# Kernel tuning notes

Hardware: AMD Instinct MI355X
Metric: run time of the kernel (lower is better)

## Reference

```python
import jax, jax.numpy as jnp
import numpy as np
from jax.scipy.special import erfinv

N_CHUNKS = 64
D = 128          # input_dim
O = 256          # output_dim
B = 4096         # batch (batch_last)
P = D // 2       # number of 2D pairs

def get_borders_cdf_grid(n):
    # CDF (Gaussian-quantile) spaced grid borders; clip probs to keep endpoints finite
    p = jnp.clip(jnp.arange(n + 1, dtype=jnp.float32) / n, 0.5 / n, 1.0 - 0.5 / n)
    return jnp.sqrt(2.0) * erfinv(2.0 * p - 1.0)

BORDERS = get_borders_cdf_grid(N_CHUNKS)  # (n_chunks+1,)


def setup_inputs() -> dict:
    key = jax.random.key(0)
    ks = jax.random.split(key, 5)
    s = 1.0 / np.sqrt(D)
    return {
        "x": jax.random.normal(ks[0], (D, B), dtype=jnp.float32),
        "weight_lmKAN": jnp.ones((1,), dtype=jnp.float32),
        "apply_relu_linear": 1,
        "func_parameter": jax.random.uniform(ks[1], (N_CHUNKS + 1, N_CHUNKS + 1, O, P), minval=-s, maxval=s, dtype=jnp.float32),
        "scale_parameters": jnp.ones((D,), dtype=jnp.float32),
        "bias_parameters": jnp.zeros((D,), dtype=jnp.float32),
        "W_linear": jax.random.uniform(ks[2], (O, D), minval=-s, maxval=s, dtype=jnp.float32),
        "bias_linear": jax.random.uniform(ks[3], (O,), minval=-s, maxval=s, dtype=jnp.float32),
    }


def lmkan_2d(fp, x):
    """2D bucketized grid lookup + bilinear interpolation.
    fp: (G, G, O, P) with G = n_chunks+1; x: (D, B) -> out (O, B)."""
    n = fp.shape[0] - 1
    pairs = x.reshape(P, 2, -1)                      # adjacent-channel pairs
    eps = 1e-6
    x1 = jnp.clip(pairs[:, 0], BORDERS[0], BORDERS[-1] - eps)  # (P, B)
    x2 = jnp.clip(pairs[:, 1], BORDERS[0], BORDERS[-1] - eps)
    i = jnp.clip(jnp.searchsorted(BORDERS, x1, side='right') - 1, 0, n - 1)
    j = jnp.clip(jnp.searchsorted(BORDERS, x2, side='right') - 1, 0, n - 1)
    t1 = (x1 - BORDERS[i]) / (BORDERS[i + 1] - BORDERS[i])      # (P, B) in [0,1)
    t2 = (x2 - BORDERS[j]) / (BORDERS[j + 1] - BORDERS[j])
    pidx = jnp.arange(P)[:, None]                    # (P, 1) -> broadcasts to (P, B)

    def corner(ii, jj, w):
        g = fp[ii, jj, :, pidx]                      # gather -> (P, B, O)
        return jnp.einsum('pb,pbo->ob', w, g)

    return (corner(i,     j,     (1.0 - t1) * (1.0 - t2))
          + corner(i + 1, j,     t1 * (1.0 - t2))
          + corner(i,     j + 1, (1.0 - t1) * t2)
          + corner(i + 1, j + 1, t1 * t2))


def reference(x, weight_lmKAN, apply_relu_linear, func_parameter, scale_parameters, bias_parameters, W_linear, bias_linear):
    # relu_last=True branch of the original forward
    linear_out = W_linear @ x + bias_linear[:, None]         # (O, B)
    if apply_relu_linear:
        linear_out = jax.nn.relu(linear_out)
    xs = x * scale_parameters[:, None] + bias_parameters[:, None]  # apply_scale / apply_bias
    # apply_tanh=False
    lmkan_out = lmkan_2d(func_parameter, xs)                 # (O, B)
    return 1.0 * linear_out + weight_lmKAN * lmkan_out
```

## Files before the change

### kernel.cpp

```cpp
#include <hip/hip_runtime.h>
#include <hip/hip_fp16.h>


#define NB 4096
#define ND 128
#define NO 256
#define NP 64
#define NG 65
#define PANEL 16384

__device__ __forceinline__ int bsearch65(const float* B, float v) {
  int lo = 0, hi = 65;
  while (lo < hi) {
    int m = (lo + hi) >> 1;
    if (B[m] <= v) lo = m + 1; else hi = m;
  }
  int i = lo - 1;
  return i < 0 ? 0 : (i > 63 ? 63 : i);
}

__global__ __launch_bounds__(128) void lmkan_transpose(
    const float* __restrict__ src, __half* __restrict__ dst) {
  const int panel = blockIdx.x;
  const int t = threadIdx.x;
  const float* s = src + (size_t)panel * PANEL;
  __half* d = dst + (size_t)panel * PANEL;
  const int o0 = 2 * t;
  const float4* ra = reinterpret_cast<const float4*>(s + (size_t)o0 * 64);
  const float4* rb = reinterpret_cast<const float4*>(s + (size_t)(o0 + 1) * 64);
#pragma unroll 4
  for (int pc = 0; pc < 16; ++pc) {
    float4 a = ra[pc];
    float4 b = rb[pc];
    *reinterpret_cast<__half2*>(d + (size_t)(4 * pc + 0) * NO + o0) = __floats2half2_rn(a.x, b.x);
    *reinterpret_cast<__half2*>(d + (size_t)(4 * pc + 1) * NO + o0) = __floats2half2_rn(a.y, b.y);
    *reinterpret_cast<__half2*>(d + (size_t)(4 * pc + 2) * NO + o0) = __floats2half2_rn(a.z, b.z);
    *reinterpret_cast<__half2*>(d + (size_t)(4 * pc + 3) * NO + o0) = __floats2half2_rn(a.w, b.w);
  }
}

__device__ __forceinline__ void fma8(float acc[8], float w, uint4 v) {
  const __half2* h = reinterpret_cast<const __half2*>(&v);
#pragma unroll
  for (int k = 0; k < 4; ++k) {
    float2 f = __half22float2(h[k]);
    acc[2 * k]     = fmaf(w, f.x, acc[2 * k]);
    acc[2 * k + 1] = fmaf(w, f.y, acc[2 * k + 1]);
  }
}

__global__ __launch_bounds__(256) void lmkan_gather4(
    const float* __restrict__ x, const float* __restrict__ scale,
    const float* __restrict__ biasp, const float* __restrict__ W,
    const float* __restrict__ bias_l, const float* __restrict__ wlm_p,
    const int* __restrict__ relu_p, const __half* __restrict__ fpt,
    float* __restrict__ out) {
  const int b = blockIdx.x;
  const int t = threadIdx.x;
  const int w = t >> 6;
  const int l = t & 63;
  const int h = l >> 5;
  const int L = l & 31;

  __shared__ float borders[66];
  __shared__ __align__(16) float xcol[ND];
  __shared__ int pbase[NP];
  __shared__ float4 pw[NP];
  __shared__ float lm[4][NO];

  if (t < 65) {
    float pk = fminf(fmaxf((float)t * (1.0f / 64.0f), 0.0078125f), 0.9921875f);
    borders[t] = 1.41421356237309515f * erfinvf(2.0f * pk - 1.0f);
  }
  if (t < ND) xcol[t] = x[(size_t)t * NB + b];
  __syncthreads();

  if (t < NP) {
    const int p = t;
    float x1 = xcol[2 * p]     * scale[2 * p]     + biasp[2 * p];
    float x2 = xcol[2 * p + 1] * scale[2 * p + 1] + biasp[2 * p + 1];
    const float lo = borders[0];
    const float hi = borders[64] - 1e-6f;
    x1 = fminf(fmaxf(x1, lo), hi);
    x2 = fminf(fmaxf(x2, lo), hi);
    int i = bsearch65(borders, x1);
    int j = bsearch65(borders, x2);
    float t1 = (x1 - borders[i]) / (borders[i + 1] - borders[i]);
    float t2 = (x2 - borders[j]) / (borders[j + 1] - borders[j]);
    pbase[p] = i * NG + j;
    pw[p] = make_float4((1.0f - t1) * (1.0f - t2),
                        t1 * (1.0f - t2),
                        (1.0f - t1) * t2,
                        t1 * t2);
  }
  __syncthreads();

  float acc[8] = {0, 0, 0, 0, 0, 0, 0, 0};
  const int p0 = w * 16;
#pragma unroll 8
  for (int pi = 0; pi < 16; ++pi) {
    const int p = p0 + pi;
    const int base = pbase[p] + h * NG;
    const float4 wv = pw[p];
    const float wA = h ? wv.y : wv.x;
    const float wB = h ? wv.w : wv.z;
    const __half* q = fpt + ((size_t)base * NP + p) * NO + 8 * L;
    uint4 v0 = *reinterpret_cast<const uint4*>(q);
    uint4 v1 = *reinterpret_cast<const uint4*>(q + PANEL);
    fma8(acc, wA, v0);
    fma8(acc, wB, v1);
  }
#pragma unroll
  for (int k = 0; k < 8; ++k) acc[k] += __shfl_xor(acc[k], 32, 64);
  if (l < 32) {
#pragma unroll
    for (int k = 0; k < 8; ++k) lm[w][8 * L + k] = acc[k];
  }
  __syncthreads();

  const int o = t;
  float lmsum = lm[0][o] + lm[1][o] + lm[2][o] + lm[3][o];
  const float4* wr = reinterpret_cast<const float4*>(W + (size_t)o * ND);
  const float4* xc4 = reinterpret_cast<const float4*>(xcol);
  float s = 0.0f;
#pragma unroll 8
  for (int d4 = 0; d4 < ND / 4; ++d4) {
    float4 wv = wr[d4];
    float4 xv = xc4[d4];
    s = fmaf(wv.x, xv.x, s);
    s = fmaf(wv.y, xv.y, s);
    s = fmaf(wv.z, xv.z, s);
    s = fmaf(wv.w, xv.w, s);
  }
  s += bias_l[o];
  if (relu_p[0]) s = fmaxf(s, 0.0f);
  out[(size_t)o * NB + b] = s + wlm_p[0] * lmsum;
}

__global__ __launch_bounds__(64) void lmkan_gather_direct(
    const float* __restrict__ x, const float* __restrict__ scale,
    const float* __restrict__ biasp, const float* __restrict__ W,
    const float* __restrict__ bias_l, const float* __restrict__ wlm_p,
    const int* __restrict__ relu_p, const float* __restrict__ fp,
    float* __restrict__ out) {
  const int b = blockIdx.x;
  const int t = threadIdx.x;

  __shared__ float borders[66];
  __shared__ __align__(16) float xcol[ND];
  __shared__ int pbase[NP];
  __shared__ float4 pw[NP];

  for (int k = t; k < 65; k += 64) {
    float pk = fminf(fmaxf((float)k * (1.0f / 64.0f), 0.0078125f), 0.9921875f);
    borders[k] = 1.41421356237309515f * erfinvf(2.0f * pk - 1.0f);
  }
  xcol[t]      = x[(size_t)t * NB + b];
  xcol[t + 64] = x[(size_t)(t + 64) * NB + b];
  __syncthreads();

  {
    const int p = t;
    float x1 = xcol[2 * p]     * scale[2 * p]     + biasp[2 * p];
    float x2 = xcol[2 * p + 1] * scale[2 * p + 1] + biasp[2 * p + 1];
    const float lo = borders[0];
    const float hi = borders[64] - 1e-6f;
    x1 = fminf(fmaxf(x1, lo), hi);
    x2 = fminf(fmaxf(x2, lo), hi);
    int i = bsearch65(borders, x1);
    int j = bsearch65(borders, x2);
    float t1 = (x1 - borders[i]) / (borders[i + 1] - borders[i]);
    float t2 = (x2 - borders[j]) / (borders[j + 1] - borders[j]);
    pbase[p] = i * NG + j;
    pw[p] = make_float4((1.0f - t1) * (1.0f - t2), t1 * (1.0f - t2),
                        (1.0f - t1) * t2, t1 * t2);
  }
  __syncthreads();

  float acc[4] = {0, 0, 0, 0};
  for (int p = 0; p < NP; ++p) {
    int base = pbase[p];
    float4 wv = pw[p];
#pragma unroll
    for (int k = 0; k < 4; ++k) {
      size_t r = ((size_t)base * NO + (4 * t + k)) * NP + p;
      acc[k] += wv.x * fp[r] + wv.y * fp[r + 65 * PANEL] +
                wv.z * fp[r + PANEL] + wv.w * fp[r + 66 * PANEL];
    }
  }

  const float wlm = wlm_p[0];
  const int rl = relu_p[0];
  const float4* xc4 = reinterpret_cast<const float4*>(xcol);
#pragma unroll
  for (int k = 0; k < 4; ++k) {
    const int o = 4 * t + k;
    const float4* wr = reinterpret_cast<const float4*>(W + (size_t)o * ND);
    float s = 0.0f;
#pragma unroll 8
    for (int d4 = 0; d4 < ND / 4; ++d4) {
      float4 wv = wr[d4];
      float4 xv = xc4[d4];
      s = fmaf(wv.x, xv.x, s);
      s = fmaf(wv.y, xv.y, s);
      s = fmaf(wv.z, xv.z, s);
      s = fmaf(wv.w, xv.w, s);
    }
    s += bias_l[o];
    if (rl) s = fmaxf(s, 0.0f);
    out[(size_t)o * NB + b] = s + wlm * acc[k];
  }
}

extern "C" void kernel_launch(void* const* d_in, const int* in_sizes, int n_in,
                              void* d_out, int out_size, void* d_ws, size_t ws_size,
                              hipStream_t stream) {
  const float* x     = reinterpret_cast<const float*>(d_in[0]);
  const float* wlm   = reinterpret_cast<const float*>(d_in[1]);
  const int*   relu  = reinterpret_cast<const int*>(d_in[2]);
  const float* fp    = reinterpret_cast<const float*>(d_in[3]);
  const float* scale = reinterpret_cast<const float*>(d_in[4]);
  const float* biasp = reinterpret_cast<const float*>(d_in[5]);
  const float* W     = reinterpret_cast<const float*>(d_in[6]);
  const float* bl    = reinterpret_cast<const float*>(d_in[7]);
  float* out = reinterpret_cast<float*>(d_out);

  const size_t need = (size_t)NG * NG * PANEL * sizeof(__half);
  if (ws_size >= need) {
    __half* fpt = reinterpret_cast<__half*>(d_ws);
    lmkan_transpose<<<NG * NG, 128, 0, stream>>>(fp, fpt);
    lmkan_gather4<<<NB, 256, 0, stream>>>(x, scale, biasp, W, bl, wlm, relu, fpt, out);
  } else {
    lmkan_gather_direct<<<NB, 64, 0, stream>>>(x, scale, biasp, W, bl, wlm, relu, fp, out);
  }
}
```

Baseline: 227.1 us.

## Relayout fp16 grid so pair corners are adjacent; split linear into tiled GEMM kernel

The transpose kernel now stages each panel through LDS and writes the fp16 table in a (i, p, j, o) layout. In that layout the i/i+1 corners sit at a fixed stride and the j/j+1 corners are contiguous, so each lane loads one 1 KB row span covering both j corners instead of scattered panels. The dense linear layer moves out of the per-sample gather kernel into a separate kernel that tiles 32 batch columns in LDS and reuses W rows across them, then accumulates into the output. This removes the per-sample W reload, at the cost of an extra launch and a read-modify-write pass over the output.

```diff
diff --git a/kernel.cpp b/kernel.cpp
--- a/kernel.cpp
+++ b/kernel.cpp
@@ -8,6 +8,9 @@
 #define NP 64
 #define NG 65
 #define PANEL 16384
+#define ROW2OFF (64 * 65 * 256)
+
+union Pack8 { __half h[8]; uint4 v; };
 
 __device__ __forceinline__ int bsearch65(const float* B, float v) {
   int lo = 0, hi = 65;
@@ -19,23 +22,35 @@
   return i < 0 ? 0 : (i > 63 ? 63 : i);
 }
 
-__global__ __launch_bounds__(128) void lmkan_transpose(
+__global__ __launch_bounds__(256) void lmkan_transpose2(
     const float* __restrict__ src, __half* __restrict__ dst) {
   const int panel = blockIdx.x;
-  const int t = threadIdx.x;
-  const float* s = src + (size_t)panel * PANEL;
-  __half* d = dst + (size_t)panel * PANEL;
-  const int o0 = 2 * t;
-  const float4* ra = reinterpret_cast<const float4*>(s + (size_t)o0 * 64);
-  const float4* rb = reinterpret_cast<const float4*>(s + (size_t)(o0 + 1) * 64);
-#pragma unroll 4
-  for (int pc = 0; pc < 16; ++pc) {
-    float4 a = ra[pc];
-    float4 b = rb[pc];
-    *reinterpret_cast<__half2*>(d + (size_t)(4 * pc + 0) * NO + o0) = __floats2half2_rn(a.x, b.x);
-    *reinterpret_cast<__half2*>(d + (size_t)(4 * pc + 1) * NO + o0) = __floats2half2_rn(a.y, b.y);
-    *reinterpret_cast<__half2*>(d + (size_t)(4 * pc + 2) * NO + o0) = __floats2half2_rn(a.z, b.z);
-    *reinterpret_cast<__half2*>(d + (size_t)(4 * pc + 3) * NO + o0) = __floats2half2_rn(a.w, b.w);
+  const int i = panel / NG, j = panel % NG;
+  const int t = threadIdx.x;
+  __shared__ __half lds[256 * 72];
+
+  const float4* s4 = reinterpret_cast<const float4*>(src + (size_t)panel * PANEL);
+#pragma unroll
+  for (int k = 0; k < 16; ++k) {
+    int idx4 = t + 256 * k;
+    float4 v = s4[idx4];
+    int o = idx4 >> 4;
+    int p0 = (idx4 & 15) * 4;
+    union { __half2 h2[2]; uint2 u; } pk;
+    pk.h2[0] = __floats2half2_rn(v.x, v.y);
+    pk.h2[1] = __floats2half2_rn(v.z, v.w);
+    *reinterpret_cast<uint2*>(&lds[o * 72 + p0]) = pk.u;
+  }
+  __syncthreads();
+
+  const int p = t & 63, oc = t >> 6;
+  __half* dbase = dst + (((size_t)(i * 64 + p) * NG + j) * NO) + oc * 64;
+#pragma unroll
+  for (int s = 0; s < 8; ++s) {
+    Pack8 pk;
+#pragma unroll
+    for (int r = 0; r < 8; ++r) pk.h[r] = lds[(oc * 64 + 8 * s + r) * 72 + p];
+    *reinterpret_cast<uint4*>(dbase + 8 * s) = pk.v;
   }
 }
 
@@ -51,20 +66,18 @@
 
 __global__ __launch_bounds__(256) void lmkan_gather4(
     const float* __restrict__ x, const float* __restrict__ scale,
-    const float* __restrict__ biasp, const float* __restrict__ W,
-    const float* __restrict__ bias_l, const float* __restrict__ wlm_p,
-    const int* __restrict__ relu_p, const __half* __restrict__ fpt,
-    float* __restrict__ out) {
+    const float* __restrict__ biasp, const float* __restrict__ wlm_p,
+    const __half* __restrict__ fpt, float* __restrict__ out) {
   const int b = blockIdx.x;
   const int t = threadIdx.x;
   const int w = t >> 6;
   const int l = t & 63;
-  const int h = l >> 5;
-  const int L = l & 31;
+  const int sideJ = l >> 5;
+  const int o0 = 8 * (l & 31);
 
   __shared__ float borders[66];
-  __shared__ __align__(16) float xcol[ND];
-  __shared__ int pbase[NP];
+  __shared__ float xcol[ND];
+  __shared__ int pbaseEl[NP];
   __shared__ float4 pw[NP];
   __shared__ float lm[4][NO];
 
@@ -87,7 +100,7 @@
     int j = bsearch65(borders, x2);
     float t1 = (x1 - borders[i]) / (borders[i + 1] - borders[i]);
     float t2 = (x2 - borders[j]) / (borders[j + 1] - borders[j]);
-    pbase[p] = i * NG + j;
+    pbaseEl[p] = ((i * 64 + p) * NG + j) * NO;
     pw[p] = make_float4((1.0f - t1) * (1.0f - t2),
                         t1 * (1.0f - t2),
                         (1.0f - t1) * t2,
@@ -97,16 +110,15 @@
 
   float acc[8] = {0, 0, 0, 0, 0, 0, 0, 0};
   const int p0 = w * 16;
-#pragma unroll 8
+#pragma unroll 4
   for (int pi = 0; pi < 16; ++pi) {
     const int p = p0 + pi;
-    const int base = pbase[p] + h * NG;
     const float4 wv = pw[p];
-    const float wA = h ? wv.y : wv.x;
-    const float wB = h ? wv.w : wv.z;
-    const __half* q = fpt + ((size_t)base * NP + p) * NO + 8 * L;
+    const float wA = sideJ ? wv.z : wv.x;
+    const float wB = sideJ ? wv.w : wv.y;
+    const __half* q = fpt + pbaseEl[p] + 8 * l;
     uint4 v0 = *reinterpret_cast<const uint4*>(q);
-    uint4 v1 = *reinterpret_cast<const uint4*>(q + PANEL);
+    uint4 v1 = *reinterpret_cast<const uint4*>(q + ROW2OFF);
     fma8(acc, wA, v0);
     fma8(acc, wB, v1);
   }
@@ -114,27 +126,58 @@
   for (int k = 0; k < 8; ++k) acc[k] += __shfl_xor(acc[k], 32, 64);
   if (l < 32) {
 #pragma unroll
-    for (int k = 0; k < 8; ++k) lm[w][8 * L + k] = acc[k];
+    for (int k = 0; k < 8; ++k) lm[w][o0 + k] = acc[k];
   }
   __syncthreads();
 
   const int o = t;
   float lmsum = lm[0][o] + lm[1][o] + lm[2][o] + lm[3][o];
-  const float4* wr = reinterpret_cast<const float4*>(W + (size_t)o * ND);
-  const float4* xc4 = reinterpret_cast<const float4*>(xcol);
-  float s = 0.0f;
+  out[(size_t)o * NB + b] = wlm_p[0] * lmsum;
+}
+
+__global__ __launch_bounds__(256) void lmkan_linear(
+    const float* __restrict__ x, const float* __restrict__ W,
+    const float* __restrict__ bias_l, const int* __restrict__ relu_p,
+    float* __restrict__ out) {
+  const int b0 = blockIdx.x * 32;
+  const int t = threadIdx.x;
+  __shared__ __align__(16) float xs[32 * 132];
+
+#pragma unroll
+  for (int k = 0; k < 16; ++k) {
+    int idx = t + 256 * k;
+    int d = idx >> 5, bb = idx & 31;
+    xs[bb * 132 + d] = x[(size_t)d * NB + b0 + bb];
+  }
+  __syncthreads();
+
+  float acc[32];
+#pragma unroll
+  for (int bb = 0; bb < 32; ++bb) acc[bb] = 0.0f;
+
+  const float4* W4 = reinterpret_cast<const float4*>(W + (size_t)t * ND);
 #pragma unroll 8
-  for (int d4 = 0; d4 < ND / 4; ++d4) {
-    float4 wv = wr[d4];
-    float4 xv = xc4[d4];
-    s = fmaf(wv.x, xv.x, s);
-    s = fmaf(wv.y, xv.y, s);
-    s = fmaf(wv.z, xv.z, s);
-    s = fmaf(wv.w, xv.w, s);
-  }
-  s += bias_l[o];
-  if (relu_p[0]) s = fmaxf(s, 0.0f);
-  out[(size_t)o * NB + b] = s + wlm_p[0] * lmsum;
+  for (int d4 = 0; d4 < 32; ++d4) {
+    float4 wv = W4[d4];
+#pragma unroll
+    for (int bb = 0; bb < 32; ++bb) {
+      float4 xv = *reinterpret_cast<const float4*>(&xs[bb * 132 + d4 * 4]);
+      acc[bb] = fmaf(wv.x, xv.x, acc[bb]);
+      acc[bb] = fmaf(wv.y, xv.y, acc[bb]);
+      acc[bb] = fmaf(wv.z, xv.z, acc[bb]);
+      acc[bb] = fmaf(wv.w, xv.w, acc[bb]);
+    }
+  }
+
+  const float bias = bias_l[t];
+  const int rl = relu_p[0];
+  float* orow = out + (size_t)t * NB + b0;
+#pragma unroll
+  for (int bb = 0; bb < 32; ++bb) {
+    float v = acc[bb] + bias;
+    if (rl) v = fmaxf(v, 0.0f);
+    orow[bb] += v;
+  }
 }
 
 __global__ __launch_bounds__(64) void lmkan_gather_direct(
@@ -228,8 +271,9 @@
   const size_t need = (size_t)NG * NG * PANEL * sizeof(__half);
   if (ws_size >= need) {
     __half* fpt = reinterpret_cast<__half*>(d_ws);
-    lmkan_transpose<<<NG * NG, 128, 0, stream>>>(fp, fpt);
-    lmkan_gather4<<<NB, 256, 0, stream>>>(x, scale, biasp, W, bl, wlm, relu, fpt, out);
+    lmkan_transpose2<<<NG * NG, 256, 0, stream>>>(fp, fpt);
+    lmkan_gather4<<<NB, 256, 0, stream>>>(x, scale, biasp, wlm, fpt, out);
+    lmkan_linear<<<NB / 32, 256, 0, stream>>>(x, W, bl, relu, out);
   } else {
     lmkan_gather_direct<<<NB, 64, 0, stream>>>(x, scale, biasp, W, bl, wlm, relu, fp, out);
   }
```

After: 195.1 us. 14.1% less time.
